# Performance work log

Measured on AMD Instinct MI355X. Metric: run time of the kernel, lower is better.

## Reference

```python
import jax, jax.numpy as jnp
import numpy as np

DIM = 512
HEADS = 8
DIM_HEAD = 64
INNER = HEADS * DIM_HEAD  # 512
SCALE = DIM_HEAD ** -0.5
LN_EPS = 1e-5


def setup_inputs() -> dict:
    key = jax.random.key(0)
    k1, k2, k3, k4 = jax.random.split(key, 4)
    b, p, n = 4, 64, 256
    x = jax.random.normal(k1, (b, p, n, DIM), dtype=jnp.float32)
    ln_g = jnp.ones((DIM,), jnp.float32)
    ln_b = jnp.zeros((DIM,), jnp.float32)
    # stored as [in, out] for x @ W
    w_qkv = jax.random.normal(k2, (DIM, 3 * INNER), jnp.float32) * (DIM ** -0.5)
    w_out = jax.random.normal(k3, (INNER, DIM), jnp.float32) * (INNER ** -0.5)
    b_out = jnp.zeros((DIM,), jnp.float32)
    return {"x": x, "ln_g": ln_g, "ln_b": ln_b, "w_qkv": w_qkv,
            "w_out": w_out, "b_out": b_out}


def reference(x, ln_g, ln_b, w_qkv, w_out, b_out):
    b, p, n, _ = x.shape
    # LayerNorm over last dim
    mu = jnp.mean(x, axis=-1, keepdims=True)
    var = jnp.mean(jnp.square(x - mu), axis=-1, keepdims=True)
    xn = (x - mu) * jax.lax.rsqrt(var + LN_EPS) * ln_g + ln_b
    # QKV projection (no bias)
    qkv = xn @ w_qkv                                   # [b,p,n,3*INNER]
    q, k, v = jnp.split(qkv, 3, axis=-1)
    def to_heads(t):
        return t.reshape(b, p, n, HEADS, DIM_HEAD).transpose(0, 1, 3, 2, 4)
    q, k, v = to_heads(q), to_heads(k), to_heads(v)    # [b,p,h,n,d]
    dots = jnp.einsum('bphnd,bphmd->bphnm', q, k) * SCALE
    attn = jax.nn.softmax(dots, axis=-1)
    out = jnp.einsum('bphnm,bphmd->bphnd', attn, v)    # [b,p,h,n,d]
    out = out.transpose(0, 1, 3, 2, 4).reshape(b, p, n, INNER)
    return out @ w_out + b_out
```

## Files before the change

kernel.cpp:

```cpp
#include <hip/hip_runtime.h>
#include <stdint.h>

#define DIMD 512
#define HEADS 8
#define DHEAD 64
#define NSEQ 256
#define NGRP 256
#define TRIPLE 1536
#define ATT_SCALE 0.125f

typedef float f32x4 __attribute__((ext_vector_type(4)));
typedef _Float16 half8 __attribute__((ext_vector_type(8)));
typedef _Float16 half4 __attribute__((ext_vector_type(4)));

#define GLD16(gp, lp) __builtin_amdgcn_global_load_lds( \
    (const __attribute__((address_space(1))) void*)(gp), \
    (__attribute__((address_space(3))) void*)(lp), 16, 0, 0)
#define BAR() __builtin_amdgcn_s_barrier()
#define VMW(n) asm volatile("s_waitcnt vmcnt(" #n ")" ::: "memory")

__global__ __launch_bounds__(256) void k_wconv(const float* __restrict__ wq,
                                               const float* __restrict__ wo,
                                               _Float16* __restrict__ wtq,
                                               _Float16* __restrict__ wto) {
  int id = blockIdx.x * 256 + threadIdx.x;
  if (id < DIMD * TRIPLE) {
    int k = id / TRIPLE, n = id % TRIPLE;
    wtq[n * DIMD + k] = (_Float16)wq[id];
  } else {
    int j = id - DIMD * TRIPLE;
    int k = j / DIMD, n = j % DIMD;
    wto[n * DIMD + k] = (_Float16)wo[j];
  }
}

__global__ __launch_bounds__(256) void k_ln(const float* __restrict__ x,
                                            const float* __restrict__ g,
                                            const float* __restrict__ b,
                                            _Float16* __restrict__ xn) {
  int row = blockIdx.x * 4 + (threadIdx.x >> 6);
  int lane = threadIdx.x & 63;
  const float* xr = x + (size_t)row * DIMD + lane * 8;
  float v[8];
  *(f32x4*)(v)     = *(const f32x4*)(xr);
  *(f32x4*)(v + 4) = *(const f32x4*)(xr + 4);
  float s = 0.f, ss = 0.f;
#pragma unroll
  for (int j = 0; j < 8; ++j) { s += v[j]; ss += v[j] * v[j]; }
#pragma unroll
  for (int m = 1; m < 64; m <<= 1) { s += __shfl_xor(s, m); ss += __shfl_xor(ss, m); }
  float mean = s * (1.f / DIMD);
  float var  = ss * (1.f / DIMD) - mean * mean;
  float rstd = rsqrtf(var + 1e-5f);
  const float* gp = g + lane * 8;
  const float* bp = b + lane * 8;
  half8 o;
#pragma unroll
  for (int j = 0; j < 8; ++j) o[j] = (_Float16)((v[j] - mean) * rstd * gp[j] + bp[j]);
  *(half8*)(xn + (size_t)row * DIMD + lane * 8) = o;
}

template <int N, int LDA>
__global__ __launch_bounds__(512, 2) void k_gemm8(const _Float16* __restrict__ A,
                                                  const _Float16* __restrict__ BT,
                                                  _Float16* __restrict__ C) {
  constexpr int NT = N / 256;
  constexpr int NWG = 256 * NT;
  constexpr int CPX = NWG / 8;
  int b = blockIdx.x;
  int logical = (b & 7) * CPX + (b >> 3);
  int mt = logical / NT, nt = logical % NT;
  int m0 = mt * 256, n0 = nt * 256;

  int tid = threadIdx.x, lane = tid & 63, w = tid >> 6;
  int wrow = w >> 2, wcol = w & 3;
  int l15 = lane & 15, lg = lane >> 4;
  const int sr = lane >> 3;
  const int ss = lane & 7;

  __shared__ _Float16 S[65536];

  f32x4 acc[8][4] = {};
  half8 af[4][2], bf0[2][2], bf1[2][2];

  auto stageA = [&](int d, int kt, int hf) {
#pragma unroll
    for (int cc = 0; cc < 2; ++cc) {
      int rbase = cc * 128 + hf * 64 + w * 8;
      const _Float16* g = A + (size_t)(m0 + rbase + sr) * LDA + kt * 64 + (ss ^ sr) * 8;
      _Float16* l = &S[d * 32768 + rbase * 64];
      GLD16(g, l);
    }
  };
  auto stageB = [&](int d, int kt, int hf) {
#pragma unroll
    for (int cc = 0; cc < 2; ++cc) {
      int i = cc * 64 + w * 8;
      int rbase = (i >> 5) * 64 + hf * 32 + (i & 31);
      const _Float16* g = BT + (size_t)(n0 + rbase + sr) * 512 + kt * 64 + (ss ^ sr) * 8;
      _Float16* l = &S[d * 32768 + 16384 + rbase * 64];
      GLD16(g, l);
    }
  };
  auto loadA = [&](int c, int mh) {
#pragma unroll
    for (int mf = 0; mf < 4; ++mf) {
      int row = wrow * 128 + mh * 64 + mf * 16 + l15;
#pragma unroll
      for (int kk = 0; kk < 2; ++kk) {
        int byte = row * 128 + ((kk * 64 + lg * 16) ^ ((row & 7) << 4));
        af[mf][kk] = *(const half8*)((const char*)&S[c * 32768] + byte);
      }
    }
  };
  auto loadB = [&](int c, int nh, half8 (&bf)[2][2]) {
#pragma unroll
    for (int nf = 0; nf < 2; ++nf) {
      int row = wcol * 64 + nh * 32 + nf * 16 + l15;
#pragma unroll
      for (int kk = 0; kk < 2; ++kk) {
        int byte = row * 128 + ((kk * 64 + lg * 16) ^ ((row & 7) << 4));
        bf[nf][kk] = *(const half8*)((const char*)&S[c * 32768 + 16384] + byte);
      }
    }
  };
  auto quad = [&](int mh, int nh, half8 (&bf)[2][2]) {
    __builtin_amdgcn_s_setprio(1);
#pragma unroll
    for (int mf = 0; mf < 4; ++mf)
#pragma unroll
      for (int nf = 0; nf < 2; ++nf)
#pragma unroll
        for (int kk = 0; kk < 2; ++kk)
          acc[mh * 4 + mf][nh * 2 + nf] = __builtin_amdgcn_mfma_f32_16x16x32_f16(
              af[mf][kk], bf[nf][kk], acc[mh * 4 + mf][nh * 2 + nf], 0, 0, 0);
    __builtin_amdgcn_s_setprio(0);
  };

  stageA(0, 0, 0); stageB(0, 0, 0); stageB(0, 0, 1); stageA(0, 0, 1);
  VMW(4); BAR();

  for (int t = 0; t < 7; ++t) {
    int c = t & 1, d = c ^ 1;
    loadA(c, 0); loadB(c, 0, bf0);
    stageA(d, t + 1, 0);
    BAR(); quad(0, 0, bf0); VMW(4); BAR();
    loadB(c, 1, bf1);
    stageB(d, t + 1, 0);
    BAR(); quad(0, 1, bf1); VMW(4); BAR();
    loadA(c, 1);
    stageB(d, t + 1, 1);
    BAR(); quad(1, 0, bf0); BAR();
    stageA(d, t + 1, 1);
    BAR(); quad(1, 1, bf1); VMW(4); BAR();
  }
  {
    loadA(1, 0); loadB(1, 0, bf0);
    BAR(); quad(0, 0, bf0); VMW(2); BAR();
    loadB(1, 1, bf1);
    BAR(); quad(0, 1, bf1); VMW(0); BAR();
    loadA(1, 1);
    BAR(); quad(1, 0, bf0); BAR();
    BAR(); quad(1, 1, bf1); BAR();
  }

#pragma unroll
  for (int mq = 0; mq < 8; ++mq)
#pragma unroll
    for (int nq = 0; nq < 4; ++nq)
#pragma unroll
      for (int r = 0; r < 4; ++r) {
        int row = m0 + wrow * 128 + (mq >> 2) * 64 + (mq & 3) * 16 + lg * 4 + r;
        int col = n0 + wcol * 64 + (nq >> 1) * 32 + (nq & 1) * 16 + l15;
        C[(size_t)row * N + col] = (_Float16)acc[mq][nq][r];
      }
}

template <int N, int LDA, bool WITH_BIAS>
__global__ __launch_bounds__(256, 2) void k_gemm(const _Float16* __restrict__ A,
                                                 const _Float16* __restrict__ BT,
                                                 _Float16* __restrict__ Ch,
                                                 float* __restrict__ Cf,
                                                 const float* __restrict__ bias) {
  constexpr int NT = N / 128;
  constexpr int NWG = 512 * NT;
  constexpr int CPX = NWG / 8;
  int bsw = (blockIdx.x & 7) * CPX + (blockIdx.x >> 3);
  int mt = bsw / NT, nt = bsw % NT;
  int m0 = mt * 128, n0 = nt * 128;
  int tid = threadIdx.x, lane = tid & 63, w = tid >> 6;
  int wr = w >> 1, wc = w & 1;
  int l15 = lane & 15, lg = lane >> 4;
  __shared__ _Float16 Asm[128 * 64];
  __shared__ _Float16 Bsm[128 * 64];
  f32x4 acc[4][4] = {};
  const int rA = lane >> 3;
  const int cA = (lane & 7) * 8;

  for (int ks = 0; ks < 8; ++ks) {
    int k0 = ks * 64;
#pragma unroll
    for (int i = 0; i < 4; ++i) {
      int r0 = w * 32 + i * 8;
      GLD16(A  + (size_t)(m0 + r0 + rA) * LDA + k0 + cA, &Asm[r0 * 64]);
      GLD16(BT + (size_t)(n0 + r0 + rA) * 512 + k0 + cA, &Bsm[r0 * 64]);
    }
    __syncthreads();
#pragma unroll
    for (int kk = 0; kk < 2; ++kk) {
      int co = kk * 32 + lg * 8;
      half8 a[4], b[4];
#pragma unroll
      for (int m = 0; m < 4; ++m) a[m] = *(const half8*)&Asm[(wr * 64 + m * 16 + l15) * 64 + co];
#pragma unroll
      for (int n = 0; n < 4; ++n) b[n] = *(const half8*)&Bsm[(wc * 64 + n * 16 + l15) * 64 + co];
#pragma unroll
      for (int m = 0; m < 4; ++m)
#pragma unroll
        for (int n = 0; n < 4; ++n)
          acc[m][n] = __builtin_amdgcn_mfma_f32_16x16x32_f16(a[m], b[n], acc[m][n], 0, 0, 0);
    }
    __syncthreads();
  }

  int rowb = m0 + wr * 64 + lg * 4;
  int colb = n0 + wc * 64 + l15;
  float bb[4];
  if constexpr (WITH_BIAS) {
#pragma unroll
    for (int n = 0; n < 4; ++n) bb[n] = bias[colb + n * 16];
  }
#pragma unroll
  for (int m = 0; m < 4; ++m)
#pragma unroll
    for (int n = 0; n < 4; ++n)
#pragma unroll
      for (int r = 0; r < 4; ++r) {
        size_t idx = (size_t)(rowb + m * 16 + r) * N + colb + n * 16;
        if constexpr (WITH_BIAS)
          Cf[idx] = acc[m][n][r] + bb[n];
        else
          Ch[idx] = (_Float16)acc[m][n][r];
      }
}

__global__ __launch_bounds__(256, 2) void k_attn(_Float16* __restrict__ qkv) {
  int g = blockIdx.x >> 3, h = blockIdx.x & 7;
  int tid = threadIdx.x, lane = tid & 63, w = tid >> 6;
  int l15 = lane & 15, lg = lane >> 4;
  __shared__ _Float16 Kt[64 * 72];
  __shared__ _Float16 Vt[64 * 72];
  __shared__ _Float16 Pl[4][64 * 72];
  const size_t base = (size_t)g * NSEQ * TRIPLE;

  half8 qf[4][2];
#pragma unroll
  for (int nq = 0; nq < 4; ++nq)
#pragma unroll
    for (int kd = 0; kd < 2; ++kd)
      qf[nq][kd] = *(const half8*)&qkv[base + (size_t)(w * 64 + nq * 16 + l15) * TRIPLE
                                       + h * 64 + kd * 32 + lg * 8];

  f32x4 oacc[4][4] = {};
  float mrun[4], lrun[4];
#pragma unroll
  for (int nq = 0; nq < 4; ++nq) { mrun[nq] = -3.0e38f; lrun[nq] = 0.f; }

  for (int kt = 0; kt < 4; ++kt) {
    __syncthreads();
#pragma unroll
    for (int i = 0; i < 2; ++i) {
      int idx = tid + i * 256;
      int key = idx >> 3, dh0 = (idx & 7) * 8;
      half8 kv = *(const half8*)&qkv[base + (size_t)(kt * 64 + key) * TRIPLE + 512 + h * 64 + dh0];
      *(half8*)&Kt[key * 72 + dh0] = kv;
      half8 vv = *(const half8*)&qkv[base + (size_t)(kt * 64 + key) * TRIPLE + 1024 + h * 64 + dh0];
#pragma unroll
      for (int j = 0; j < 8; ++j) Vt[(dh0 + j) * 72 + key] = vv[j];
    }
    __syncthreads();

    f32x4 st[4][4] = {};
#pragma unroll
    for (int kd = 0; kd < 2; ++kd) {
      int co = kd * 32 + lg * 8;
      half8 kf[4];
#pragma unroll
      for (int mk = 0; mk < 4; ++mk) kf[mk] = *(const half8*)&Kt[(mk * 16 + l15) * 72 + co];
#pragma unroll
      for (int mk = 0; mk < 4; ++mk)
#pragma unroll
        for (int nq = 0; nq < 4; ++nq)
          st[mk][nq] = __builtin_amdgcn_mfma_f32_16x16x32_f16(kf[mk], qf[nq][kd], st[mk][nq], 0, 0, 0);
    }

    float alpha[4];
#pragma unroll
    for (int nq = 0; nq < 4; ++nq) {
      float pm = -3.0e38f;
#pragma unroll
      for (int mk = 0; mk < 4; ++mk)
#pragma unroll
        for (int r = 0; r < 4; ++r) {
          st[mk][nq][r] *= ATT_SCALE;
          pm = fmaxf(pm, st[mk][nq][r]);
        }
      pm = fmaxf(pm, __shfl_xor(pm, 16));
      pm = fmaxf(pm, __shfl_xor(pm, 32));
      float mn = fmaxf(mrun[nq], pm);
      alpha[nq] = __expf(mrun[nq] - mn);
      mrun[nq] = mn;
      float ps = 0.f;
#pragma unroll
      for (int mk = 0; mk < 4; ++mk) {
        half4 p4;
#pragma unroll
        for (int r = 0; r < 4; ++r) {
          float e = __expf(st[mk][nq][r] - mn);
          ps += e;
          p4[r] = (_Float16)e;
        }
        *(half4*)&Pl[w][(nq * 16 + l15) * 72 + mk * 16 + lg * 4] = p4;
      }
      ps += __shfl_xor(ps, 16);
      ps += __shfl_xor(ps, 32);
      lrun[nq] = lrun[nq] * alpha[nq] + ps;
    }

#pragma unroll
    for (int mp = 0; mp < 4; ++mp)
#pragma unroll
      for (int r = 0; r < 4; ++r) {
        float av = __shfl(alpha[mp], lg * 4 + r);
#pragma unroll
        for (int nd = 0; nd < 4; ++nd) oacc[mp][nd][r] *= av;
      }

    __syncthreads();

#pragma unroll
    for (int kp = 0; kp < 2; ++kp) {
      int co = kp * 32 + lg * 8;
      half8 pf[4], vf[4];
#pragma unroll
      for (int mp = 0; mp < 4; ++mp) pf[mp] = *(const half8*)&Pl[w][(mp * 16 + l15) * 72 + co];
#pragma unroll
      for (int nd = 0; nd < 4; ++nd) vf[nd] = *(const half8*)&Vt[(nd * 16 + l15) * 72 + co];
#pragma unroll
      for (int mp = 0; mp < 4; ++mp)
#pragma unroll
        for (int nd = 0; nd < 4; ++nd)
          oacc[mp][nd] = __builtin_amdgcn_mfma_f32_16x16x32_f16(pf[mp], vf[nd], oacc[mp][nd], 0, 0, 0);
    }
  }

#pragma unroll
  for (int mp = 0; mp < 4; ++mp)
#pragma unroll
    for (int r = 0; r < 4; ++r) {
      float li = 1.f / __shfl(lrun[mp], lg * 4 + r);
      int q = w * 64 + mp * 16 + lg * 4 + r;
#pragma unroll
      for (int nd = 0; nd < 4; ++nd)
        qkv[base + (size_t)q * TRIPLE + h * 64 + nd * 16 + l15] =
            (_Float16)(oacc[mp][nd][r] * li);
    }
}

extern "C" void kernel_launch(void* const* d_in, const int* in_sizes, int n_in,
                              void* d_out, int out_size, void* d_ws, size_t ws_size,
                              hipStream_t stream) {
  const float* x     = (const float*)d_in[0];
  const float* ln_g  = (const float*)d_in[1];
  const float* ln_b  = (const float*)d_in[2];
  const float* w_qkv = (const float*)d_in[3];
  const float* w_out = (const float*)d_in[4];
  const float* b_out = (const float*)d_in[5];

  char* ws = (char*)d_ws;
  _Float16* qkv = (_Float16*)ws;
  _Float16* wtq = (_Float16*)(ws + 201326592ull);
  _Float16* wto = (_Float16*)(ws + 201326592ull + 1572864ull);
  _Float16* xn  = (_Float16*)d_out;
  float* out    = (float*)d_out;

  k_wconv<<<4096, 256, 0, stream>>>(w_qkv, w_out, wtq, wto);
  k_ln<<<16384, 256, 0, stream>>>(x, ln_g, ln_b, xn);
  k_gemm8<TRIPLE, DIMD><<<1536, 512, 0, stream>>>(xn, wtq, qkv);
  k_attn<<<2048, 256, 0, stream>>>(qkv);
  k_gemm<DIMD, TRIPLE, true><<<2048, 256, 0, stream>>>(qkv, wto, nullptr, out, b_out);
}
```

Before: 306.7 us.

## Merge prep kernels, reuse 256x256 GEMM for output projection, async K staging

Merges the weight-convert and LayerNorm kernels into one launch. Replaces the 128x128 output-projection GEMM with the pipelined 256x256 k_gemm8 template, which gains an fp32+bias epilogue. In attention, K tiles are now staged with direct global-to-LDS loads into an XOR-swizzled layout instead of register round trips. The aim is fewer launches, more data reuse per tile in the output GEMM, and cheaper K staging. The trade-off is that only 512 workgroups are left for the output GEMM.

```diff
diff --git a/kernel.cpp b/kernel.cpp
--- a/kernel.cpp
+++ b/kernel.cpp
@@ -19,26 +19,28 @@
 #define BAR() __builtin_amdgcn_s_barrier()
 #define VMW(n) asm volatile("s_waitcnt vmcnt(" #n ")" ::: "memory")
 
-__global__ __launch_bounds__(256) void k_wconv(const float* __restrict__ wq,
-                                               const float* __restrict__ wo,
-                                               _Float16* __restrict__ wtq,
-                                               _Float16* __restrict__ wto) {
-  int id = blockIdx.x * 256 + threadIdx.x;
-  if (id < DIMD * TRIPLE) {
-    int k = id / TRIPLE, n = id % TRIPLE;
-    wtq[n * DIMD + k] = (_Float16)wq[id];
-  } else {
-    int j = id - DIMD * TRIPLE;
-    int k = j / DIMD, n = j % DIMD;
-    wto[n * DIMD + k] = (_Float16)wo[j];
-  }
-}
-
-__global__ __launch_bounds__(256) void k_ln(const float* __restrict__ x,
-                                            const float* __restrict__ g,
-                                            const float* __restrict__ b,
-                                            _Float16* __restrict__ xn) {
-  int row = blockIdx.x * 4 + (threadIdx.x >> 6);
+__global__ __launch_bounds__(256) void k_pre(const float* __restrict__ x,
+                                             const float* __restrict__ g,
+                                             const float* __restrict__ b,
+                                             const float* __restrict__ wq,
+                                             const float* __restrict__ wo,
+                                             _Float16* __restrict__ xn,
+                                             _Float16* __restrict__ wtq,
+                                             _Float16* __restrict__ wto) {
+  int bid = blockIdx.x;
+  if (bid < 4096) {
+    int id = bid * 256 + threadIdx.x;
+    if (id < DIMD * TRIPLE) {
+      int k = id / TRIPLE, n = id % TRIPLE;
+      wtq[n * DIMD + k] = (_Float16)wq[id];
+    } else {
+      int j = id - DIMD * TRIPLE;
+      int k = j / DIMD, n = j % DIMD;
+      wto[n * DIMD + k] = (_Float16)wo[j];
+    }
+    return;
+  }
+  int row = (bid - 4096) * 4 + (threadIdx.x >> 6);
   int lane = threadIdx.x & 63;
   const float* xr = x + (size_t)row * DIMD + lane * 8;
   float v[8];
@@ -60,10 +62,12 @@
   *(half8*)(xn + (size_t)row * DIMD + lane * 8) = o;
 }
 
-template <int N, int LDA>
+template <int N, int LDA, bool F32OUT>
 __global__ __launch_bounds__(512, 2) void k_gemm8(const _Float16* __restrict__ A,
                                                   const _Float16* __restrict__ BT,
-                                                  _Float16* __restrict__ C) {
+                                                  _Float16* __restrict__ Ch,
+                                                  float* __restrict__ Cf,
+                                                  const float* __restrict__ bias) {
   constexpr int NT = N / 256;
   constexpr int NWG = 256 * NT;
   constexpr int CPX = NWG / 8;
@@ -87,9 +91,9 @@
 #pragma unroll
     for (int cc = 0; cc < 2; ++cc) {
       int rbase = cc * 128 + hf * 64 + w * 8;
-      const _Float16* g = A + (size_t)(m0 + rbase + sr) * LDA + kt * 64 + (ss ^ sr) * 8;
+      const _Float16* gp = A + (size_t)(m0 + rbase + sr) * LDA + kt * 64 + (ss ^ sr) * 8;
       _Float16* l = &S[d * 32768 + rbase * 64];
-      GLD16(g, l);
+      GLD16(gp, l);
     }
   };
   auto stageB = [&](int d, int kt, int hf) {
@@ -97,9 +101,9 @@
     for (int cc = 0; cc < 2; ++cc) {
       int i = cc * 64 + w * 8;
       int rbase = (i >> 5) * 64 + hf * 32 + (i & 31);
-      const _Float16* g = BT + (size_t)(n0 + rbase + sr) * 512 + kt * 64 + (ss ^ sr) * 8;
+      const _Float16* gp = BT + (size_t)(n0 + rbase + sr) * 512 + kt * 64 + (ss ^ sr) * 8;
       _Float16* l = &S[d * 32768 + 16384 + rbase * 64];
-      GLD16(g, l);
+      GLD16(gp, l);
     }
   };
   auto loadA = [&](int c, int mh) {
@@ -164,6 +168,12 @@
     BAR(); quad(1, 1, bf1); BAR();
   }
 
+  float bb[4];
+  if constexpr (F32OUT) {
+#pragma unroll
+    for (int nq = 0; nq < 4; ++nq)
+      bb[nq] = bias[n0 + wcol * 64 + (nq >> 1) * 32 + (nq & 1) * 16 + l15];
+  }
 #pragma unroll
   for (int mq = 0; mq < 8; ++mq)
 #pragma unroll
@@ -172,75 +182,10 @@
       for (int r = 0; r < 4; ++r) {
         int row = m0 + wrow * 128 + (mq >> 2) * 64 + (mq & 3) * 16 + lg * 4 + r;
         int col = n0 + wcol * 64 + (nq >> 1) * 32 + (nq & 1) * 16 + l15;
-        C[(size_t)row * N + col] = (_Float16)acc[mq][nq][r];
-      }
-}
-
-template <int N, int LDA, bool WITH_BIAS>
-__global__ __launch_bounds__(256, 2) void k_gemm(const _Float16* __restrict__ A,
-                                                 const _Float16* __restrict__ BT,
-                                                 _Float16* __restrict__ Ch,
-                                                 float* __restrict__ Cf,
-                                                 const float* __restrict__ bias) {
-  constexpr int NT = N / 128;
-  constexpr int NWG = 512 * NT;
-  constexpr int CPX = NWG / 8;
-  int bsw = (blockIdx.x & 7) * CPX + (blockIdx.x >> 3);
-  int mt = bsw / NT, nt = bsw % NT;
-  int m0 = mt * 128, n0 = nt * 128;
-  int tid = threadIdx.x, lane = tid & 63, w = tid >> 6;
-  int wr = w >> 1, wc = w & 1;
-  int l15 = lane & 15, lg = lane >> 4;
-  __shared__ _Float16 Asm[128 * 64];
-  __shared__ _Float16 Bsm[128 * 64];
-  f32x4 acc[4][4] = {};
-  const int rA = lane >> 3;
-  const int cA = (lane & 7) * 8;
-
-  for (int ks = 0; ks < 8; ++ks) {
-    int k0 = ks * 64;
-#pragma unroll
-    for (int i = 0; i < 4; ++i) {
-      int r0 = w * 32 + i * 8;
-      GLD16(A  + (size_t)(m0 + r0 + rA) * LDA + k0 + cA, &Asm[r0 * 64]);
-      GLD16(BT + (size_t)(n0 + r0 + rA) * 512 + k0 + cA, &Bsm[r0 * 64]);
-    }
-    __syncthreads();
-#pragma unroll
-    for (int kk = 0; kk < 2; ++kk) {
-      int co = kk * 32 + lg * 8;
-      half8 a[4], b[4];
-#pragma unroll
-      for (int m = 0; m < 4; ++m) a[m] = *(const half8*)&Asm[(wr * 64 + m * 16 + l15) * 64 + co];
-#pragma unroll
-      for (int n = 0; n < 4; ++n) b[n] = *(const half8*)&Bsm[(wc * 64 + n * 16 + l15) * 64 + co];
-#pragma unroll
-      for (int m = 0; m < 4; ++m)
-#pragma unroll
-        for (int n = 0; n < 4; ++n)
-          acc[m][n] = __builtin_amdgcn_mfma_f32_16x16x32_f16(a[m], b[n], acc[m][n], 0, 0, 0);
-    }
-    __syncthreads();
-  }
-
-  int rowb = m0 + wr * 64 + lg * 4;
-  int colb = n0 + wc * 64 + l15;
-  float bb[4];
-  if constexpr (WITH_BIAS) {
-#pragma unroll
-    for (int n = 0; n < 4; ++n) bb[n] = bias[colb + n * 16];
-  }
-#pragma unroll
-  for (int m = 0; m < 4; ++m)
-#pragma unroll
-    for (int n = 0; n < 4; ++n)
-#pragma unroll
-      for (int r = 0; r < 4; ++r) {
-        size_t idx = (size_t)(rowb + m * 16 + r) * N + colb + n * 16;
-        if constexpr (WITH_BIAS)
-          Cf[idx] = acc[m][n][r] + bb[n];
+        if constexpr (F32OUT)
+          Cf[(size_t)row * N + col] = acc[mq][nq][r] + bb[nq];
         else
-          Ch[idx] = (_Float16)acc[m][n][r];
+          Ch[(size_t)row * N + col] = (_Float16)acc[mq][nq][r];
       }
 }
 
@@ -248,7 +193,7 @@
   int g = blockIdx.x >> 3, h = blockIdx.x & 7;
   int tid = threadIdx.x, lane = tid & 63, w = tid >> 6;
   int l15 = lane & 15, lg = lane >> 4;
-  __shared__ _Float16 Kt[64 * 72];
+  __shared__ _Float16 Kt[64 * 64];
   __shared__ _Float16 Vt[64 * 72];
   __shared__ _Float16 Pl[4][64 * 72];
   const size_t base = (size_t)g * NSEQ * TRIPLE;
@@ -266,27 +211,39 @@
 #pragma unroll
   for (int nq = 0; nq < 4; ++nq) { mrun[nq] = -3.0e38f; lrun[nq] = 0.f; }
 
+  const int srow = lane >> 3;
+  const int sslot = lane & 7;
+
   for (int kt = 0; kt < 4; ++kt) {
     __syncthreads();
+#pragma unroll
+    for (int rnd = 0; rnd < 2; ++rnd) {
+      int rbase = rnd * 32 + w * 8;
+      const _Float16* gp = &qkv[base + (size_t)(kt * 64 + rbase + srow) * TRIPLE
+                                + 512 + h * 64 + (sslot ^ srow) * 8];
+      GLD16(gp, &Kt[rbase * 64]);
+    }
 #pragma unroll
     for (int i = 0; i < 2; ++i) {
       int idx = tid + i * 256;
       int key = idx >> 3, dh0 = (idx & 7) * 8;
-      half8 kv = *(const half8*)&qkv[base + (size_t)(kt * 64 + key) * TRIPLE + 512 + h * 64 + dh0];
-      *(half8*)&Kt[key * 72 + dh0] = kv;
       half8 vv = *(const half8*)&qkv[base + (size_t)(kt * 64 + key) * TRIPLE + 1024 + h * 64 + dh0];
 #pragma unroll
       for (int j = 0; j < 8; ++j) Vt[(dh0 + j) * 72 + key] = vv[j];
     }
+    VMW(0);
     __syncthreads();
 
     f32x4 st[4][4] = {};
 #pragma unroll
     for (int kd = 0; kd < 2; ++kd) {
-      int co = kd * 32 + lg * 8;
       half8 kf[4];
 #pragma unroll
-      for (int mk = 0; mk < 4; ++mk) kf[mk] = *(const half8*)&Kt[(mk * 16 + l15) * 72 + co];
+      for (int mk = 0; mk < 4; ++mk) {
+        int r = mk * 16 + l15;
+        int byte = r * 128 + ((kd * 64 + lg * 16) ^ ((r & 7) << 4));
+        kf[mk] = *(const half8*)((const char*)Kt + byte);
+      }
 #pragma unroll
       for (int mk = 0; mk < 4; ++mk)
 #pragma unroll
@@ -384,9 +341,8 @@
   _Float16* xn  = (_Float16*)d_out;
   float* out    = (float*)d_out;
 
-  k_wconv<<<4096, 256, 0, stream>>>(w_qkv, w_out, wtq, wto);
-  k_ln<<<16384, 256, 0, stream>>>(x, ln_g, ln_b, xn);
-  k_gemm8<TRIPLE, DIMD><<<1536, 512, 0, stream>>>(xn, wtq, qkv);
+  k_pre<<<20480, 256, 0, stream>>>(x, ln_g, ln_b, w_qkv, w_out, xn, wtq, wto);
+  k_gemm8<TRIPLE, DIMD, false><<<1536, 512, 0, stream>>>(xn, wtq, qkv, nullptr, nullptr);
   k_attn<<<2048, 256, 0, stream>>>(qkv);
-  k_gemm<DIMD, TRIPLE, true><<<2048, 256, 0, stream>>>(qkv, wto, nullptr, out, b_out);
+  k_gemm8<DIMD, TRIPLE, true><<<512, 512, 0, stream>>>(qkv, wto, nullptr, out, b_out);
 }
```

After: 288.2 us. 6.0% less time.
